# Kernel tuning notes

Measured on AMD Instinct MI355X. Metric: run time of the kernel, lower is better.

Reference implementation:

```python
import jax, jax.numpy as jnp
import numpy as np

B, LQ, LK, D, H = 8, 512, 512, 512, 128

def setup_inputs() -> dict:
    key = jax.random.key(0)
    k1, k2, k3, k4, k5 = jax.random.split(key, 5)
    qs = jax.random.normal(k1, (B, LQ, D), dtype=jnp.float32)
    ks = jax.random.normal(k2, (B, LK, D), dtype=jnp.float32)
    # Dense kernels: flax Dense stores kernel as [in_features, out_features]
    Wq = jax.random.normal(k3, (D, H), dtype=jnp.float32) / np.sqrt(D)
    Wk = jax.random.normal(k4, (D, H), dtype=jnp.float32) / np.sqrt(D)
    wv = jax.random.normal(k5, (H,), dtype=jnp.float32) / np.sqrt(H)
    return {"qs": qs, "ks": ks, "Wq": Wq, "Wk": Wk, "wv": wv}

def reference(qs, ks, Wq, Wk, wv):
    # Project queries and keys into the shared hidden space: [B,Lq,H], [B,Lk,H]
    q = jnp.einsum("bqd,dh->bqh", qs, Wq)
    k = jnp.einsum("bkd,dh->bkh", ks, Wk)
    # Broadcast-add -> tanh -> linear reduce over H: scores [B,Lq,Lk]
    feats = jnp.tanh(q[:, :, None, :] + k[:, None, :, :])  # [B,Lq,Lk,H]
    return jnp.einsum("bqkh,h->bqk", feats, wv)
```

## Files before the change

### kernel.cpp

```cpp
#include <hip/hip_runtime.h>
#include <hip/hip_bf16.h>
#include <cstdint>

#define B_   8
#define LQ_  512
#define LK_  512
#define D_   512
#define H_   128

typedef __attribute__((ext_vector_type(8))) short  short8;
typedef __attribute__((ext_vector_type(4))) float  float4v;

#define TANH_C 2.8853900817779268f

__device__ __forceinline__ short bf16rne(float x) {
  uint32_t u = __float_as_uint(x);
  return (short)((u + 0x7fffu + ((u >> 16) & 1u)) >> 16);
}

__device__ __forceinline__ float fast_tanh(float x) {
  float e = __builtin_amdgcn_exp2f(x * TANH_C);
  return 1.0f - 2.0f * __builtin_amdgcn_rcpf(e + 1.0f);
}

__global__ __launch_bounds__(256) void prep_kernel(
    const float* __restrict__ Wq, const float* __restrict__ Wk,
    short* __restrict__ WqF, short* __restrict__ WkF) {
  int g = blockIdx.x * 256 + threadIdx.x;
  int m = g >> 13;
  int r = g & 8191;
  int l  = r & 63;
  int kb = (r >> 6) & 15;
  int nt = r >> 10;
  int col = nt * 16 + (l & 15);
  int k0  = kb * 32 + ((l >> 4) << 3);
  const float* W = m ? Wk : Wq;
  short8 f;
#pragma unroll
  for (int j = 0; j < 8; ++j) f[j] = bf16rne(W[(k0 + j) * H_ + col]);
  ((short8*)(m ? WkF : WqF))[r] = f;
}

__global__ __launch_bounds__(256) void proj_kernel(
    const float* __restrict__ qs, const float* __restrict__ ks,
    const short* __restrict__ WqF, const short* __restrict__ WkF,
    float* __restrict__ qp, float* __restrict__ kp) {
  int blk  = blockIdx.x;
  int wave = threadIdx.x >> 6;
  int l    = threadIdx.x & 63;
  int grow = blk * 16;
  int m    = (grow >= 4096) ? 1 : 0;
  int r0   = grow - (m ? 4096 : 0);
  const float*  A  = m ? ks : qs;
  const short8* BF = (const short8*)(m ? WkF : WqF);
  float* out = m ? kp : qp;

  float4v acc[2];
  acc[0] = (float4v){0.f, 0.f, 0.f, 0.f};
  acc[1] = (float4v){0.f, 0.f, 0.f, 0.f};

  int quad = l >> 4;
  int arow = r0 + (l & 15);
  const float* aptr = A + (size_t)arow * D_ + quad * 8;
  int t0 = wave * 2;

#pragma unroll 4
  for (int kb = 0; kb < 16; ++kb) {
    float4v a0 = *(const float4v*)(aptr + kb * 32);
    float4v a1 = *(const float4v*)(aptr + kb * 32 + 4);
    short8 af;
#pragma unroll
    for (int j = 0; j < 4; ++j) { af[j] = bf16rne(a0[j]); af[j + 4] = bf16rne(a1[j]); }
#pragma unroll
    for (int tt = 0; tt < 2; ++tt) {
      short8 bf = BF[((t0 + tt) * 16 + kb) * 64 + l];
      acc[tt] = __builtin_amdgcn_mfma_f32_16x16x32_bf16(af, bf, acc[tt], 0, 0, 0);
    }
  }

#pragma unroll
  for (int tt = 0; tt < 2; ++tt)
#pragma unroll
    for (int r = 0; r < 4; ++r) {
      int row = r0 + quad * 4 + r;
      int col = (t0 + tt) * 16 + (l & 15);
      out[(size_t)row * H_ + col] = fast_tanh(acc[tt][r]);
    }
}

__global__ __launch_bounds__(256) void score_kernel(
    const float* __restrict__ qp, const float* __restrict__ kp,
    const float* __restrict__ wv, float* __restrict__ out) {
  __shared__ float qt[64 * 68];
  __shared__ float kt[32 * 68];

  int b = blockIdx.z, qtile = blockIdx.y, ktile = blockIdx.x;
  int t = threadIdx.x;
  int tx = t & 15, ty = t >> 4;

  const float* qbase = qp + (size_t)(b * LQ_ + qtile * 64) * H_;
  const float* kbase = kp + (size_t)(b * LK_ + ktile * 32) * H_;

  float acc[4][2];
#pragma unroll
  for (int i = 0; i < 4; ++i)
#pragma unroll
    for (int j = 0; j < 2; ++j) acc[i][j] = 0.f;

  int lr = t >> 4, lc = t & 15;

  for (int hc = 0; hc < 2; ++hc) {
    __syncthreads();
#pragma unroll
    for (int s = 0; s < 4; ++s) {
      int row = lr + 16 * s;
      *(float4v*)&qt[row * 68 + lc * 4] =
          *(const float4v*)&qbase[row * H_ + hc * 64 + lc * 4];
    }
#pragma unroll
    for (int s = 0; s < 2; ++s) {
      int row = lr + 16 * s;
      *(float4v*)&kt[row * 68 + lc * 4] =
          *(const float4v*)&kbase[row * H_ + hc * 64 + lc * 4];
    }
    __syncthreads();

    for (int h0 = 0; h0 < 64; h0 += 4) {
      float4v qv[4], kv[2];
#pragma unroll
      for (int i = 0; i < 4; ++i) qv[i] = *(const float4v*)&qt[(ty + 16 * i) * 68 + h0];
#pragma unroll
      for (int j = 0; j < 2; ++j) kv[j] = *(const float4v*)&kt[(tx + 16 * j) * 68 + h0];
      float w[4];
#pragma unroll
      for (int u = 0; u < 4; ++u) w[u] = wv[hc * 64 + h0 + u];

#pragma unroll
      for (int i = 0; i < 4; ++i)
#pragma unroll
        for (int j = 0; j < 2; ++j)
#pragma unroll
          for (int u = 0; u < 4; ++u) {
            float ta  = qv[i][u], tb = kv[j][u];
            float num = ta + tb;
            float den = fmaf(ta, tb, 1.0f);
            float r   = __builtin_amdgcn_rcpf(den);
            acc[i][j] = fmaf(w[u], num * r, acc[i][j]);
          }
    }
  }

  size_t ob = (size_t)(b * LQ_ + qtile * 64) * LK_ + ktile * 32;
#pragma unroll
  for (int i = 0; i < 4; ++i)
#pragma unroll
    for (int j = 0; j < 2; ++j)
      out[ob + (size_t)(ty + 16 * i) * LK_ + tx + 16 * j] = acc[i][j];
}

extern "C" void kernel_launch(void* const* d_in, const int* in_sizes, int n_in,
                              void* d_out, int out_size, void* d_ws, size_t ws_size,
                              hipStream_t stream) {
  const float* qs = (const float*)d_in[0];
  const float* ks = (const float*)d_in[1];
  const float* Wq = (const float*)d_in[2];
  const float* Wk = (const float*)d_in[3];
  const float* wv = (const float*)d_in[4];
  float* out = (float*)d_out;

  char* ws = (char*)d_ws;
  short* WqF = (short*)ws;
  short* WkF = (short*)(ws + (128 << 10));
  float* qp  = (float*)(ws + (256 << 10));
  float* kp  = (float*)(ws + (256 << 10) + (2 << 20));

  prep_kernel<<<64, 256, 0, stream>>>(Wq, Wk, WqF, WkF);
  proj_kernel<<<512, 256, 0, stream>>>(qs, ks, WqF, WkF, qp, kp);
  score_kernel<<<dim3(16, 8, 8), 256, 0, stream>>>(qp, kp, wv, out);
}
```

Before: 121.7 us.

## Rewrite tanh-sum as exp-domain reciprocal sum with packed vector FMAs

The projection now stores exp(2x) instead of tanh(x). The score kernel uses tanh(a+b) = 1 - 2/(1+e^{2a}e^{2b}), which replaces the add/multiply/rcp/fma chain with one fma, one rcp and one fma per element. The weight sum W0 is added once at the end. Accumulation uses 4-wide vector FMAs so the compiler can emit packed float ops. The risk is that exp overflows for large projections, giving inf in the denominator; rcp then returns 0, which still yields the correct limit. Each thread also recomputes the sum of wv.

```diff
diff --git a/kernel.cpp b/kernel.cpp
--- a/kernel.cpp
+++ b/kernel.cpp
@@ -16,11 +16,6 @@
 __device__ __forceinline__ short bf16rne(float x) {
   uint32_t u = __float_as_uint(x);
   return (short)((u + 0x7fffu + ((u >> 16) & 1u)) >> 16);
-}
-
-__device__ __forceinline__ float fast_tanh(float x) {
-  float e = __builtin_amdgcn_exp2f(x * TANH_C);
-  return 1.0f - 2.0f * __builtin_amdgcn_rcpf(e + 1.0f);
 }
 
 __global__ __launch_bounds__(256) void prep_kernel(
@@ -84,7 +79,7 @@
     for (int r = 0; r < 4; ++r) {
       int row = r0 + quad * 4 + r;
       int col = (t0 + tt) * 16 + (l & 15);
-      out[(size_t)row * H_ + col] = fast_tanh(acc[tt][r]);
+      out[(size_t)row * H_ + col] = __builtin_amdgcn_exp2f(acc[tt][r] * TANH_C);
     }
 }
 
@@ -101,11 +96,15 @@
   const float* qbase = qp + (size_t)(b * LQ_ + qtile * 64) * H_;
   const float* kbase = kp + (size_t)(b * LK_ + ktile * 32) * H_;
 
-  float acc[4][2];
+  float W0 = 0.f;
+  for (int h = 0; h < H_; ++h) W0 += wv[h];
+
+  float4v acc4[4][2];
+  const float4v ones = (float4v){1.f, 1.f, 1.f, 1.f};
 #pragma unroll
   for (int i = 0; i < 4; ++i)
 #pragma unroll
-    for (int j = 0; j < 2; ++j) acc[i][j] = 0.f;
+    for (int j = 0; j < 2; ++j) acc4[i][j] = (float4v){0.f, 0.f, 0.f, 0.f};
 
   int lr = t >> 4, lc = t & 15;
 
@@ -131,22 +130,21 @@
       for (int i = 0; i < 4; ++i) qv[i] = *(const float4v*)&qt[(ty + 16 * i) * 68 + h0];
 #pragma unroll
       for (int j = 0; j < 2; ++j) kv[j] = *(const float4v*)&kt[(tx + 16 * j) * 68 + h0];
-      float w[4];
-#pragma unroll
-      for (int u = 0; u < 4; ++u) w[u] = wv[hc * 64 + h0 + u];
+      const float* wp = wv + hc * 64 + h0;
+      float4v w4 = (float4v){-2.f * wp[0], -2.f * wp[1], -2.f * wp[2], -2.f * wp[3]};
 
 #pragma unroll
       for (int i = 0; i < 4; ++i)
 #pragma unroll
-        for (int j = 0; j < 2; ++j)
-#pragma unroll
-          for (int u = 0; u < 4; ++u) {
-            float ta  = qv[i][u], tb = kv[j][u];
-            float num = ta + tb;
-            float den = fmaf(ta, tb, 1.0f);
-            float r   = __builtin_amdgcn_rcpf(den);
-            acc[i][j] = fmaf(w[u], num * r, acc[i][j]);
-          }
+        for (int j = 0; j < 2; ++j) {
+          float4v den = __builtin_elementwise_fma(qv[i], kv[j], ones);
+          float4v r;
+          r[0] = __builtin_amdgcn_rcpf(den[0]);
+          r[1] = __builtin_amdgcn_rcpf(den[1]);
+          r[2] = __builtin_amdgcn_rcpf(den[2]);
+          r[3] = __builtin_amdgcn_rcpf(den[3]);
+          acc4[i][j] = __builtin_elementwise_fma(w4, r, acc4[i][j]);
+        }
     }
   }
 
@@ -154,8 +152,11 @@
 #pragma unroll
   for (int i = 0; i < 4; ++i)
 #pragma unroll
-    for (int j = 0; j < 2; ++j)
-      out[ob + (size_t)(ty + 16 * i) * LK_ + tx + 16 * j] = acc[i][j];
+    for (int j = 0; j < 2; ++j) {
+      float4v a = acc4[i][j];
+      out[ob + (size_t)(ty + 16 * i) * LK_ + tx + 16 * j] =
+          W0 + ((a[0] + a[1]) + (a[2] + a[3]));
+    }
 }
 
 extern "C" void kernel_launch(void* const* d_in, const int* in_sizes, int n_in,
```

Measured after the change: 112.6 us. 1.08x faster.
